# Performance work log

Measured on AMD Instinct MI355X. Metric: run time of the kernel, lower is better.

The kernel has to match this reference:

```python
import jax, jax.numpy as jnp
import numpy as np

N = 1024        # nodes; B == N required by the source's broadcasting
C2 = 64         # 2 * in_channels (x feature dim)
E = 64          # embed_dim
ALPHA = 0.2     # leaky relu negative slope
NEG = -1e12     # mask fill value from source


def setup_inputs() -> dict:
    key = jax.random.key(0)
    k1, k2, k3, k4, k5 = jax.random.split(key, 5)
    x = jax.random.normal(k1, (N, N, C2), dtype=jnp.float32)
    adj = (jax.random.uniform(k2, (N, N)) > 0.9).astype(jnp.float32)
    gain = 1.414
    W = jax.random.uniform(k3, (C2, E), jnp.float32, -1.0, 1.0) * (gain * np.sqrt(6.0 / (C2 + E)))
    a = jax.random.uniform(k4, (E, 1), jnp.float32, -1.0, 1.0) * (gain * np.sqrt(6.0 / (E + 1)))
    b = jax.random.normal(k5, (E,), dtype=jnp.float32) * 0.02
    return {"x": x, "adj": adj, "W": W, "a": a, "b": b}


def reference(x, adj, W, a, b):
    # x: [B, N, 2C] with B == N; W: [2C, E]
    wx = jnp.einsum('bnc,ce->bne', x, W)                    # [B, N, E]
    # per-node scalar attention logit, squeeze(-1) -> [B, N]
    s = jnp.squeeze(jax.nn.leaky_relu(wx, ALPHA) @ a, -1)   # [B, N]
    # adjacency masking: [B,N] + [N,N] broadcasts to [N,N] since B == N
    scores = s + jnp.where(adj > 0.0, 0.0, NEG)             # [N, N]
    att = jax.nn.softmax(scores, axis=-1)                   # [N, N]
    # 2-D attention broadcast over batch: out[b] = att @ wx[b]
    out = jnp.einsum('ij,bje->bie', att, wx) + b            # [B, N, E]
    return out
```

## Files before the change

### kernel.cpp

```cpp
#include <hip/hip_runtime.h>
#include <stdint.h>

#define N_NODES 1024
#define C2v 64
#define EMB 64
#define ALPHA 0.2f
#define NEG_FILL (-1e12f)

typedef __attribute__((ext_vector_type(8))) short short8v;
typedef __attribute__((ext_vector_type(4))) float float4v;

static __device__ __forceinline__ short f2bf(float f) {
    unsigned u = __builtin_bit_cast(unsigned, f);
    u = (u + 0x7FFFu + ((u >> 16) & 1u)) >> 16;
    return (short)(unsigned short)u;
}

__global__ __launch_bounds__(256) void k_att(const float* __restrict__ x,
                                             const float* __restrict__ adj,
                                             const float* __restrict__ W,
                                             const float* __restrict__ a,
                                             unsigned short* __restrict__ att) {
    __shared__ float s_lds[N_NODES];
    __shared__ float red[8];

    const int i   = blockIdx.x;
    const int tid = threadIdx.x;
    const int w   = tid >> 6;
    const int l   = tid & 63;
    const int g   = l >> 4;
    const int m   = l & 15;

    short8v wfrag[4][2];
#pragma unroll
    for (int nt = 0; nt < 4; ++nt)
#pragma unroll
        for (int ks = 0; ks < 2; ++ks) {
            short8v v;
#pragma unroll
            for (int ii = 0; ii < 8; ++ii)
                v[ii] = f2bf(W[(ks * 32 + g * 8 + ii) * EMB + nt * 16 + m]);
            wfrag[nt][ks] = v;
        }
    float afrag[4];
#pragma unroll
    for (int nt = 0; nt < 4; ++nt) afrag[nt] = a[nt * 16 + m];

    const float* xi = x + (size_t)i * N_NODES * C2v;

    for (int jt = 0; jt < N_NODES / 64; ++jt) {
        const int j0 = jt * 64 + w * 16;
        float4v acc[4];
#pragma unroll
        for (int nt = 0; nt < 4; ++nt) acc[nt] = (float4v)0.0f;

#pragma unroll
        for (int ks = 0; ks < 2; ++ks) {
            const float* p = xi + (size_t)(j0 + m) * C2v + ks * 32 + g * 8;
            float4v lo = *(const float4v*)p;
            float4v hi = *(const float4v*)(p + 4);
            short8v afr;
            afr[0] = f2bf(lo[0]); afr[1] = f2bf(lo[1]);
            afr[2] = f2bf(lo[2]); afr[3] = f2bf(lo[3]);
            afr[4] = f2bf(hi[0]); afr[5] = f2bf(hi[1]);
            afr[6] = f2bf(hi[2]); afr[7] = f2bf(hi[3]);
#pragma unroll
            for (int nt = 0; nt < 4; ++nt)
                acc[nt] = __builtin_amdgcn_mfma_f32_16x16x32_bf16(
                    afr, wfrag[nt][ks], acc[nt], 0, 0, 0);
        }
#pragma unroll
        for (int r = 0; r < 4; ++r) {
            float v = 0.f;
#pragma unroll
            for (int nt = 0; nt < 4; ++nt) {
                float t = acc[nt][r];
                t = (t > 0.f) ? t : (ALPHA * t);
                v += t * afrag[nt];
            }
            v += __shfl_xor(v, 1);
            v += __shfl_xor(v, 2);
            v += __shfl_xor(v, 4);
            v += __shfl_xor(v, 8);
            if (m == 0) s_lds[j0 + g * 4 + r] = v;
        }
    }
    __syncthreads();

    const float* adjrow = adj + (size_t)i * N_NODES;
    float sc[4];
    float lmax = -3.4e38f;
#pragma unroll
    for (int q = 0; q < 4; ++q) {
        int j = tid + q * 256;
        float v = s_lds[j] + (adjrow[j] > 0.f ? 0.f : NEG_FILL);
        sc[q] = v;
        lmax = fmaxf(lmax, v);
    }
#pragma unroll
    for (int d = 1; d < 64; d <<= 1) lmax = fmaxf(lmax, __shfl_xor(lmax, d));
    if (l == 0) red[w] = lmax;
    __syncthreads();
    const float M = fmaxf(fmaxf(red[0], red[1]), fmaxf(red[2], red[3]));

    float ex[4];
    float lsum = 0.f;
#pragma unroll
    for (int q = 0; q < 4; ++q) {
        ex[q] = __expf(sc[q] - M);
        lsum += ex[q];
    }
#pragma unroll
    for (int d = 1; d < 64; d <<= 1) lsum += __shfl_xor(lsum, d);
    __syncthreads();
    if (l == 0) red[w] = lsum;
    __syncthreads();
    const float S = red[0] + red[1] + red[2] + red[3];
    const float inv = 1.0f / S;

    unsigned short* arow = att + (size_t)i * N_NODES;
#pragma unroll
    for (int q = 0; q < 4; ++q) {
        int j = tid + q * 256;
        arow[j] = (unsigned short)f2bf(ex[q] * inv);
    }
}

__global__ __launch_bounds__(256) void k_out(const float* __restrict__ x,
                                             const unsigned short* __restrict__ att,
                                             const float* __restrict__ W,
                                             const float* __restrict__ bias,
                                             float* __restrict__ out) {
    __shared__ __attribute__((aligned(16))) short tmp_lds[256][72];

    const int hw = blockIdx.x;
    const int L  = (hw & 7) * 512 + (hw >> 3);
    const int b  = L >> 2;
    const int it = L & 3;

    const int tid = threadIdx.x;
    const int w   = tid >> 6;
    const int l   = tid & 63;
    const int g   = l >> 4;
    const int m   = l & 15;

    float4v acc[4][4];
#pragma unroll
    for (int mt = 0; mt < 4; ++mt)
#pragma unroll
        for (int nt = 0; nt < 4; ++nt) acc[mt][nt] = (float4v)0.0f;

    const float* xb = x + (size_t)b * N_NODES * C2v;

    for (int kt = 0; kt < 16; ++kt) {
        const int j0 = kt * 64;

        short8v afr[4][2];
#pragma unroll
        for (int mt = 0; mt < 4; ++mt)
#pragma unroll
            for (int ks = 0; ks < 2; ++ks) {
                const int row = it * 256 + w * 64 + mt * 16 + m;
                afr[mt][ks] = *(const short8v*)&att[(size_t)row * N_NODES + j0 + ks * 32 + g * 8];
            }

        short8v bfr[4][2];
#pragma unroll
        for (int nt = 0; nt < 4; ++nt)
#pragma unroll
            for (int ks = 0; ks < 2; ++ks) {
                short8v v;
#pragma unroll
                for (int ii = 0; ii < 8; ++ii) {
                    const int j = j0 + ks * 32 + g * 8 + ii;
                    v[ii] = f2bf(xb[(size_t)j * C2v + nt * 16 + m]);
                }
                bfr[nt][ks] = v;
            }

#pragma unroll
        for (int mt = 0; mt < 4; ++mt)
#pragma unroll
            for (int nt = 0; nt < 4; ++nt)
#pragma unroll
                for (int ks = 0; ks < 2; ++ks)
                    acc[mt][nt] = __builtin_amdgcn_mfma_f32_16x16x32_bf16(
                        afr[mt][ks], bfr[nt][ks], acc[mt][nt], 0, 0, 0);
    }

#pragma unroll
    for (int mt = 0; mt < 4; ++mt)
#pragma unroll
        for (int nt = 0; nt < 4; ++nt)
#pragma unroll
            for (int r = 0; r < 4; ++r)
                tmp_lds[w * 64 + mt * 16 + g * 4 + r][nt * 16 + m] = f2bf(acc[mt][nt][r]);
    __syncthreads();

    short8v wfrag[4][2];
#pragma unroll
    for (int nt = 0; nt < 4; ++nt)
#pragma unroll
        for (int ks = 0; ks < 2; ++ks) {
            short8v v;
#pragma unroll
            for (int ii = 0; ii < 8; ++ii)
                v[ii] = f2bf(W[(ks * 32 + g * 8 + ii) * EMB + nt * 16 + m]);
            wfrag[nt][ks] = v;
        }
    float bfrag[4];
#pragma unroll
    for (int nt = 0; nt < 4; ++nt) bfrag[nt] = bias[nt * 16 + m];

    float4v acc2[4][4];
#pragma unroll
    for (int mt = 0; mt < 4; ++mt)
#pragma unroll
        for (int nt = 0; nt < 4; ++nt) acc2[mt][nt] = (float4v)0.0f;

#pragma unroll
    for (int mt = 0; mt < 4; ++mt)
#pragma unroll
        for (int ks = 0; ks < 2; ++ks) {
            const short8v a2 = *(const short8v*)&tmp_lds[w * 64 + mt * 16 + m][ks * 32 + g * 8];
#pragma unroll
            for (int nt = 0; nt < 4; ++nt)
                acc2[mt][nt] = __builtin_amdgcn_mfma_f32_16x16x32_bf16(
                    a2, wfrag[nt][ks], acc2[mt][nt], 0, 0, 0);
        }

#pragma unroll
    for (int mt = 0; mt < 4; ++mt)
#pragma unroll
        for (int nt = 0; nt < 4; ++nt)
#pragma unroll
            for (int r = 0; r < 4; ++r) {
                const int i = it * 256 + w * 64 + mt * 16 + g * 4 + r;
                const int e = nt * 16 + m;
                out[((size_t)b * N_NODES + i) * EMB + e] = acc2[mt][nt][r] + bfrag[nt];
            }
}

extern "C" void kernel_launch(void* const* d_in, const int* in_sizes, int n_in,
                              void* d_out, int out_size, void* d_ws, size_t ws_size,
                              hipStream_t stream) {
    const float* x    = (const float*)d_in[0];
    const float* adj  = (const float*)d_in[1];
    const float* W    = (const float*)d_in[2];
    const float* a    = (const float*)d_in[3];
    const float* bias = (const float*)d_in[4];
    float* out = (float*)d_out;
    unsigned short* att = (unsigned short*)d_ws;

    k_att<<<N_NODES, 256, 0, stream>>>(x, adj, W, a, att);
    k_out<<<4096, 256, 0, stream>>>(x, att, W, bias, out);
}
```

Baseline: 882.2 us.

## Materialize transposed bf16 wx in first kernel and consume it in output GEMM

```diff
diff --git a/kernel.cpp b/kernel.cpp
--- a/kernel.cpp
+++ b/kernel.cpp
@@ -9,18 +9,29 @@
 
 typedef __attribute__((ext_vector_type(8))) short short8v;
 typedef __attribute__((ext_vector_type(4))) float float4v;
+typedef unsigned int u32;
 
 static __device__ __forceinline__ short f2bf(float f) {
     unsigned u = __builtin_bit_cast(unsigned, f);
     u = (u + 0x7FFFu + ((u >> 16) & 1u)) >> 16;
     return (short)(unsigned short)u;
 }
-
-__global__ __launch_bounds__(256) void k_att(const float* __restrict__ x,
-                                             const float* __restrict__ adj,
-                                             const float* __restrict__ W,
-                                             const float* __restrict__ a,
-                                             unsigned short* __restrict__ att) {
+static __device__ __forceinline__ u32 pack2bf(float a, float b) {
+    return (u32)(unsigned short)f2bf(a) | ((u32)(unsigned short)f2bf(b) << 16);
+}
+static __device__ __forceinline__ void gload16(const float* g, float* l) {
+    __builtin_amdgcn_global_load_lds(
+        (const __attribute__((address_space(1))) u32*)g,
+        (__attribute__((address_space(3))) u32*)l, 16, 0, 0);
+}
+
+__global__ __launch_bounds__(256) void k_wx(const float* __restrict__ x,
+                                            const float* __restrict__ adj,
+                                            const float* __restrict__ W,
+                                            const float* __restrict__ a,
+                                            unsigned short* __restrict__ wxT,
+                                            unsigned short* __restrict__ att) {
+    __shared__ float xs[2][4096];
     __shared__ float s_lds[N_NODES];
     __shared__ float red[8];
 
@@ -48,12 +59,201 @@
 
     const float* xi = x + (size_t)i * N_NODES * C2v;
 
+    auto STAGE = [&](int jt, int buf) {
+#pragma unroll
+        for (int q = 0; q < 4; ++q) {
+            const int row  = w * 16 + q * 4 + g;
+            const int slot = m ^ (row & 7);
+            gload16(xi + (size_t)(jt * 64 + row) * C2v + slot * 4,
+                    &xs[buf][w * 1024 + q * 256]);
+        }
+    };
+
+    STAGE(0, 0);
+#pragma unroll
+    for (int jt = 0; jt < 16; ++jt) {
+        const int buf = jt & 1;
+        if (jt < 15) STAGE(jt + 1, buf ^ 1);
+        if (jt < 15) { asm volatile("s_waitcnt vmcnt(4)" ::: "memory"); }
+        else         { asm volatile("s_waitcnt vmcnt(0)" ::: "memory"); }
+        __builtin_amdgcn_sched_barrier(0);
+
+        const int j0 = jt * 64 + w * 16;
+        float4v acc[4];
+#pragma unroll
+        for (int nt = 0; nt < 4; ++nt) acc[nt] = (float4v)0.0f;
+
+#pragma unroll
+        for (int ks = 0; ks < 2; ++ks) {
+            const int slo = (ks * 8 + 2 * g) ^ (m & 7);
+            const int shi = (ks * 8 + 2 * g + 1) ^ (m & 7);
+            const float4v lo = *(const float4v*)&xs[buf][w * 1024 + m * 64 + slo * 4];
+            const float4v hi = *(const float4v*)&xs[buf][w * 1024 + m * 64 + shi * 4];
+            short8v afr;
+            afr[0] = f2bf(lo[0]); afr[1] = f2bf(lo[1]);
+            afr[2] = f2bf(lo[2]); afr[3] = f2bf(lo[3]);
+            afr[4] = f2bf(hi[0]); afr[5] = f2bf(hi[1]);
+            afr[6] = f2bf(hi[2]); afr[7] = f2bf(hi[3]);
+#pragma unroll
+            for (int nt = 0; nt < 4; ++nt)
+                acc[nt] = __builtin_amdgcn_mfma_f32_16x16x32_bf16(
+                    afr, wfrag[nt][ks], acc[nt], 0, 0, 0);
+        }
+
+#pragma unroll
+        for (int nt = 0; nt < 4; ++nt) {
+            uint2 pk;
+            pk.x = pack2bf(acc[nt][0], acc[nt][1]);
+            pk.y = pack2bf(acc[nt][2], acc[nt][3]);
+            *(uint2*)&wxT[((size_t)i * EMB + nt * 16 + m) * N_NODES + j0 + g * 4] = pk;
+        }
+
+#pragma unroll
+        for (int r = 0; r < 4; ++r) {
+            float v = 0.f;
+#pragma unroll
+            for (int nt = 0; nt < 4; ++nt) {
+                float t = acc[nt][r];
+                t = (t > 0.f) ? t : (ALPHA * t);
+                v += t * afrag[nt];
+            }
+            v += __shfl_xor(v, 1);
+            v += __shfl_xor(v, 2);
+            v += __shfl_xor(v, 4);
+            v += __shfl_xor(v, 8);
+            if (m == 0) s_lds[j0 + g * 4 + r] = v;
+        }
+    }
+    __syncthreads();
+
+    const float* adjrow = adj + (size_t)i * N_NODES;
+    float sc[4];
+    float lmax = -3.4e38f;
+#pragma unroll
+    for (int q = 0; q < 4; ++q) {
+        int j = tid + q * 256;
+        float v = s_lds[j] + (adjrow[j] > 0.f ? 0.f : NEG_FILL);
+        sc[q] = v;
+        lmax = fmaxf(lmax, v);
+    }
+#pragma unroll
+    for (int d = 1; d < 64; d <<= 1) lmax = fmaxf(lmax, __shfl_xor(lmax, d));
+    if (l == 0) red[w] = lmax;
+    __syncthreads();
+    const float M = fmaxf(fmaxf(red[0], red[1]), fmaxf(red[2], red[3]));
+
+    float ex[4];
+    float lsum = 0.f;
+#pragma unroll
+    for (int q = 0; q < 4; ++q) {
+        ex[q] = __expf(sc[q] - M);
+        lsum += ex[q];
+    }
+#pragma unroll
+    for (int d = 1; d < 64; d <<= 1) lsum += __shfl_xor(lsum, d);
+    __syncthreads();
+    if (l == 0) red[w] = lsum;
+    __syncthreads();
+    const float S = red[0] + red[1] + red[2] + red[3];
+    const float inv = 1.0f / S;
+
+    unsigned short* arow = att + (size_t)i * N_NODES;
+#pragma unroll
+    for (int q = 0; q < 4; ++q) {
+        int j = tid + q * 256;
+        arow[j] = (unsigned short)f2bf(ex[q] * inv);
+    }
+}
+
+__global__ __launch_bounds__(256) void k_out2(const unsigned short* __restrict__ wxT,
+                                              const unsigned short* __restrict__ att,
+                                              const float* __restrict__ bias,
+                                              float* __restrict__ out) {
+    const int hw = blockIdx.x;
+    const int L  = (hw & 7) * 512 + (hw >> 3);
+    const int b  = L >> 2;
+    const int it = L & 3;
+
+    const int tid = threadIdx.x;
+    const int w   = tid >> 6;
+    const int l   = tid & 63;
+    const int g   = l >> 4;
+    const int m   = l & 15;
+
+    const int i0 = it * 256 + w * 64;
+    const size_t abase = (size_t)(i0 + m) * N_NODES;
+    const size_t bbase = ((size_t)b * EMB + m) * N_NODES;
+
+    float4v acc[4][4];
+#pragma unroll
+    for (int mt = 0; mt < 4; ++mt)
+#pragma unroll
+        for (int nt = 0; nt < 4; ++nt) acc[mt][nt] = (float4v)0.0f;
+
+    for (int kt = 0; kt < 16; ++kt) {
+#pragma unroll
+        for (int ks = 0; ks < 2; ++ks) {
+            const int jc = kt * 64 + ks * 32 + g * 8;
+            short8v afr[4], bfr[4];
+#pragma unroll
+            for (int mt = 0; mt < 4; ++mt)
+                afr[mt] = *(const short8v*)&att[abase + (size_t)mt * 16 * N_NODES + jc];
+#pragma unroll
+            for (int nt = 0; nt < 4; ++nt)
+                bfr[nt] = *(const short8v*)&wxT[bbase + (size_t)nt * 16 * N_NODES + jc];
+#pragma unroll
+            for (int mt = 0; mt < 4; ++mt)
+#pragma unroll
+                for (int nt = 0; nt < 4; ++nt)
+                    acc[mt][nt] = __builtin_amdgcn_mfma_f32_16x16x32_bf16(
+                        afr[mt], bfr[nt], acc[mt][nt], 0, 0, 0);
+        }
+    }
+
+    float bv[4];
+#pragma unroll
+    for (int nt = 0; nt < 4; ++nt) bv[nt] = bias[nt * 16 + m];
+
+#pragma unroll
+    for (int mt = 0; mt < 4; ++mt)
+#pragma unroll
+        for (int nt = 0; nt < 4; ++nt)
+#pragma unroll
+            for (int r = 0; r < 4; ++r) {
+                const int i = i0 + mt * 16 + g * 4 + r;
+                out[((size_t)b * N_NODES + i) * EMB + nt * 16 + m] = acc[mt][nt][r] + bv[nt];
+            }
+}
+
+__global__ __launch_bounds__(256) void k_att_fb(const float* __restrict__ x,
+                                                const float* __restrict__ adj,
+                                                const float* __restrict__ W,
+                                                const float* __restrict__ a,
+                                                unsigned short* __restrict__ att) {
+    __shared__ float s_lds[N_NODES];
+    __shared__ float red[8];
+    const int i = blockIdx.x, tid = threadIdx.x;
+    const int w = tid >> 6, l = tid & 63, g = l >> 4, m = l & 15;
+    short8v wfrag[4][2];
+#pragma unroll
+    for (int nt = 0; nt < 4; ++nt)
+#pragma unroll
+        for (int ks = 0; ks < 2; ++ks) {
+            short8v v;
+#pragma unroll
+            for (int ii = 0; ii < 8; ++ii)
+                v[ii] = f2bf(W[(ks * 32 + g * 8 + ii) * EMB + nt * 16 + m]);
+            wfrag[nt][ks] = v;
+        }
+    float afrag[4];
+#pragma unroll
+    for (int nt = 0; nt < 4; ++nt) afrag[nt] = a[nt * 16 + m];
+    const float* xi = x + (size_t)i * N_NODES * C2v;
     for (int jt = 0; jt < N_NODES / 64; ++jt) {
         const int j0 = jt * 64 + w * 16;
         float4v acc[4];
 #pragma unroll
         for (int nt = 0; nt < 4; ++nt) acc[nt] = (float4v)0.0f;
-
 #pragma unroll
         for (int ks = 0; ks < 2; ++ks) {
             const float* p = xi + (size_t)(j0 + m) * C2v + ks * 32 + g * 8;
@@ -66,8 +266,7 @@
             afr[6] = f2bf(hi[2]); afr[7] = f2bf(hi[3]);
 #pragma unroll
             for (int nt = 0; nt < 4; ++nt)
-                acc[nt] = __builtin_amdgcn_mfma_f32_16x16x32_bf16(
-                    afr, wfrag[nt][ks], acc[nt], 0, 0, 0);
+                acc[nt] = __builtin_amdgcn_mfma_f32_16x16x32_bf16(afr, wfrag[nt][ks], acc[nt], 0, 0, 0);
         }
 #pragma unroll
         for (int r = 0; r < 4; ++r) {
@@ -78,38 +277,28 @@
                 t = (t > 0.f) ? t : (ALPHA * t);
                 v += t * afrag[nt];
             }
-            v += __shfl_xor(v, 1);
-            v += __shfl_xor(v, 2);
-            v += __shfl_xor(v, 4);
-            v += __shfl_xor(v, 8);
+            v += __shfl_xor(v, 1); v += __shfl_xor(v, 2);
+            v += __shfl_xor(v, 4); v += __shfl_xor(v, 8);
             if (m == 0) s_lds[j0 + g * 4 + r] = v;
         }
     }
     __syncthreads();
-
     const float* adjrow = adj + (size_t)i * N_NODES;
-    float sc[4];
-    float lmax = -3.4e38f;
+    float sc[4]; float lmax = -3.4e38f;
 #pragma unroll
     for (int q = 0; q < 4; ++q) {
         int j = tid + q * 256;
         float v = s_lds[j] + (adjrow[j] > 0.f ? 0.f : NEG_FILL);
-        sc[q] = v;
-        lmax = fmaxf(lmax, v);
+        sc[q] = v; lmax = fmaxf(lmax, v);
     }
 #pragma unroll
     for (int d = 1; d < 64; d <<= 1) lmax = fmaxf(lmax, __shfl_xor(lmax, d));
     if (l == 0) red[w] = lmax;
     __syncthreads();
     const float M = fmaxf(fmaxf(red[0], red[1]), fmaxf(red[2], red[3]));
-
-    float ex[4];
-    float lsum = 0.f;
-#pragma unroll
-    for (int q = 0; q < 4; ++q) {
-        ex[q] = __expf(sc[q] - M);
-        lsum += ex[q];
-    }
+    float ex[4]; float lsum = 0.f;
+#pragma unroll
+    for (int q = 0; q < 4; ++q) { ex[q] = __expf(sc[q] - M); lsum += ex[q]; }
 #pragma unroll
     for (int d = 1; d < 64; d <<= 1) lsum += __shfl_xor(lsum, d);
     __syncthreads();
@@ -117,7 +306,6 @@
     __syncthreads();
     const float S = red[0] + red[1] + red[2] + red[3];
     const float inv = 1.0f / S;
-
     unsigned short* arow = att + (size_t)i * N_NODES;
 #pragma unroll
     for (int q = 0; q < 4; ++q) {
@@ -126,44 +314,34 @@
     }
 }
 
-__global__ __launch_bounds__(256) void k_out(const float* __restrict__ x,
-                                             const unsigned short* __restrict__ att,
-                                             const float* __restrict__ W,
-                                             const float* __restrict__ bias,
-                                             float* __restrict__ out) {
+__global__ __launch_bounds__(256) void k_out_fb(const float* __restrict__ x,
+                                                const unsigned short* __restrict__ att,
+                                                const float* __restrict__ W,
+                                                const float* __restrict__ bias,
+                                                float* __restrict__ out) {
     __shared__ __attribute__((aligned(16))) short tmp_lds[256][72];
-
     const int hw = blockIdx.x;
     const int L  = (hw & 7) * 512 + (hw >> 3);
     const int b  = L >> 2;
     const int it = L & 3;
-
     const int tid = threadIdx.x;
-    const int w   = tid >> 6;
-    const int l   = tid & 63;
-    const int g   = l >> 4;
-    const int m   = l & 15;
-
+    const int w = tid >> 6, l = tid & 63, g = l >> 4, m = l & 15;
     float4v acc[4][4];
 #pragma unroll
     for (int mt = 0; mt < 4; ++mt)
 #pragma unroll
         for (int nt = 0; nt < 4; ++nt) acc[mt][nt] = (float4v)0.0f;
-
     const float* xb = x + (size_t)b * N_NODES * C2v;
-
     for (int kt = 0; kt < 16; ++kt) {
         const int j0 = kt * 64;
-
         short8v afr[4][2];
 #pragma unroll
-        for (int mt = 0; mt < 4; ++mt)
+    for (int mt = 0; mt < 4; ++mt)
 #pragma unroll
             for (int ks = 0; ks < 2; ++ks) {
                 const int row = it * 256 + w * 64 + mt * 16 + m;
                 afr[mt][ks] = *(const short8v*)&att[(size_t)row * N_NODES + j0 + ks * 32 + g * 8];
             }
-
         short8v bfr[4][2];
 #pragma unroll
         for (int nt = 0; nt < 4; ++nt)
@@ -177,7 +355,6 @@
                 }
                 bfr[nt][ks] = v;
             }
-
 #pragma unroll
         for (int mt = 0; mt < 4; ++mt)
 #pragma unroll
@@ -187,7 +364,6 @@
                     acc[mt][nt] = __builtin_amdgcn_mfma_f32_16x16x32_bf16(
                         afr[mt][ks], bfr[nt][ks], acc[mt][nt], 0, 0, 0);
     }
-
 #pragma unroll
     for (int mt = 0; mt < 4; ++mt)
 #pragma unroll
@@ -196,7 +372,6 @@
             for (int r = 0; r < 4; ++r)
                 tmp_lds[w * 64 + mt * 16 + g * 4 + r][nt * 16 + m] = f2bf(acc[mt][nt][r]);
     __syncthreads();
-
     short8v wfrag[4][2];
 #pragma unroll
     for (int nt = 0; nt < 4; ++nt)
@@ -211,13 +386,11 @@
     float bfrag[4];
 #pragma unroll
     for (int nt = 0; nt < 4; ++nt) bfrag[nt] = bias[nt * 16 + m];
-
     float4v acc2[4][4];
 #pragma unroll
     for (int mt = 0; mt < 4; ++mt)
 #pragma unroll
         for (int nt = 0; nt < 4; ++nt) acc2[mt][nt] = (float4v)0.0f;
-
 #pragma unroll
     for (int mt = 0; mt < 4; ++mt)
 #pragma unroll
@@ -225,10 +398,8 @@
             const short8v a2 = *(const short8v*)&tmp_lds[w * 64 + mt * 16 + m][ks * 32 + g * 8];
 #pragma unroll
             for (int nt = 0; nt < 4; ++nt)
-                acc2[mt][nt] = __builtin_amdgcn_mfma_f32_16x16x32_bf16(
-                    a2, wfrag[nt][ks], acc2[mt][nt], 0, 0, 0);
-        }
-
+                acc2[mt][nt] = __builtin_amdgcn_mfma_f32_16x16x32_bf16(a2, wfrag[nt][ks], acc2[mt][nt], 0, 0, 0);
+        }
 #pragma unroll
     for (int mt = 0; mt < 4; ++mt)
 #pragma unroll
@@ -236,8 +407,7 @@
 #pragma unroll
             for (int r = 0; r < 4; ++r) {
                 const int i = it * 256 + w * 64 + mt * 16 + g * 4 + r;
-                const int e = nt * 16 + m;
-                out[((size_t)b * N_NODES + i) * EMB + e] = acc2[mt][nt][r] + bfrag[nt];
+                out[((size_t)b * N_NODES + i) * EMB + nt * 16 + m] = acc2[mt][nt][r] + bfrag[nt];
             }
 }
 
@@ -250,8 +420,18 @@
     const float* a    = (const float*)d_in[3];
     const float* bias = (const float*)d_in[4];
     float* out = (float*)d_out;
-    unsigned short* att = (unsigned short*)d_ws;
-
-    k_att<<<N_NODES, 256, 0, stream>>>(x, adj, W, a, att);
-    k_out<<<4096, 256, 0, stream>>>(x, att, W, bias, out);
-}
+
+    const size_t WXT_BYTES = (size_t)N_NODES * EMB * N_NODES * 2;
+    const size_t ATT_BYTES = (size_t)N_NODES * N_NODES * 2;
+
+    if (ws_size >= WXT_BYTES + ATT_BYTES) {
+        unsigned short* wxT = (unsigned short*)d_ws;
+        unsigned short* att = (unsigned short*)((char*)d_ws + WXT_BYTES);
+        k_wx<<<N_NODES, 256, 0, stream>>>(x, adj, W, a, wxT, att);
+        k_out2<<<4096, 256, 0, stream>>>(wxT, att, bias, out);
+    } else {
+        unsigned short* att = (unsigned short*)d_ws;
+        k_att_fb<<<N_NODES, 256, 0, stream>>>(x, adj, W, a, att);
+        k_out_fb<<<4096, 256, 0, stream>>>(x, att, W, bias, out);
+    }
+}
```

After: 933.2 us. 1.06x slower.
